# Kernel tuning notes

Hardware: AMD Instinct MI355X
Metric: run time of the kernel (lower is better)

The kernel has to match this reference:

```python
import jax, jax.numpy as jnp
import numpy as np

NEG_BIG = -9e15
ALPHA = 0.2  # leakyrelu slope


def setup_inputs() -> dict:
    key = jax.random.key(0)
    k1, k2, k3, k4 = jax.random.split(key, 4)
    N, Fin, Fout = 8192, 256, 256
    input = jax.random.normal(k1, (N, Fin), dtype=jnp.float32)
    adj = jax.random.randint(k2, (N, N), 0, 2, dtype=jnp.int32)
    W = jax.random.normal(k3, (Fin, Fout), dtype=jnp.float32) * (1.0 / np.sqrt(Fin))
    a = jax.random.normal(k4, (2 * Fout, 1), dtype=jnp.float32) * (1.0 / np.sqrt(Fout))
    return {"input": input, "adj": adj, "W": W, "a": a}


def reference(input, adj, W, a):
    # h: [N, F]
    h = input @ W
    Fout = h.shape[1]
    # Fused score: e_ij = leakyrelu(h_i . a[:F] + h_j . a[F:])
    s1 = h @ a[:Fout, 0]   # [N]
    s2 = h @ a[Fout:, 0]   # [N]
    e = s1[:, None] + s2[None, :]            # [N, N]
    e = jnp.where(e >= 0, e, ALPHA * e)      # leaky relu
    e = jnp.where(adj > 0, e, NEG_BIG)       # mask
    attention = jax.nn.softmax(e, axis=1)    # row softmax
    h_prime = attention @ h                  # [N, F]
    return jax.nn.elu(h_prime)               # concat=True -> elu
```

## Files before the change

kernel.cpp:

```cpp
#include <hip/hip_runtime.h>
#include <hip/hip_bf16.h>

#define LRALPHA 0.2f
#define LOG2E 1.4426950408889634f

typedef __attribute__((ext_vector_type(8))) short frag_ab;
typedef __attribute__((ext_vector_type(4))) float frag_cd;
typedef int   iv4 __attribute__((ext_vector_type(4)));
typedef float fv4 __attribute__((ext_vector_type(4)));
typedef int   iv2 __attribute__((ext_vector_type(2)));
typedef float fv2 __attribute__((ext_vector_type(2)));
typedef unsigned int uv4 __attribute__((ext_vector_type(4)));

static __device__ __forceinline__ unsigned short f2bf(float f) {
  __hip_bfloat16 b = __float2bfloat16(f);
  unsigned short u;
  __builtin_memcpy(&u, &b, 2);
  return u;
}

#if __has_builtin(__builtin_amdgcn_exp2f)
#define EXP2F(x) __builtin_amdgcn_exp2f(x)
#else
#define EXP2F(x) exp2f(x)
#endif

static __device__ __forceinline__ unsigned cvt_pk_bf16(float lo, float hi) {
  unsigned r;
  asm("v_cvt_pk_bf16_f32 %0, %1, %2" : "=v"(r) : "v"(lo), "v"(hi));
  return r;
}

static __device__ __forceinline__ void block_sync_lds() {
  __builtin_amdgcn_sched_barrier(0);
  asm volatile("s_waitcnt lgkmcnt(0)" ::: "memory");
  __builtin_amdgcn_s_barrier();
  __builtin_amdgcn_sched_barrier(0);
}

static __device__ __forceinline__ unsigned make_w2(iv2 ca, fv2 cv,
                                                   float s1r, float mr, float& zloc) {
  float w[2];
#pragma unroll
  for (int e = 0; e < 2; ++e) {
    float ee = s1r + cv[e];
    ee = fmaxf(ee, LRALPHA * ee);
    float ww = EXP2F(ee - mr);
    ww = ca[e] ? ww : 0.f;
    zloc += ww;
    w[e] = ww;
  }
  return cvt_pk_bf16(w[0], w[1]);
}

__global__ __launch_bounds__(256, 4) void gat_hproj(
    const float* __restrict__ X, const float* __restrict__ W,
    const float* __restrict__ avec,
    float* __restrict__ s1, float* __restrict__ s2,
    unsigned short* __restrict__ hT) {
  const int tid = threadIdx.x;
  const int row0 = blockIdx.x * 16;
  const float* Xb = X + (size_t)row0 * 256;
  const int c = tid;

  float acc[16];
#pragma unroll
  for (int r = 0; r < 16; ++r) acc[r] = 0.f;

  for (int k = 0; k < 256; k += 4) {
    const float w0 = W[(k + 0) * 256 + c];
    const float w1 = W[(k + 1) * 256 + c];
    const float w2 = W[(k + 2) * 256 + c];
    const float w3 = W[(k + 3) * 256 + c];
#pragma unroll
    for (int r = 0; r < 16; ++r) {
      acc[r] = fmaf(Xb[r * 256 + k + 0], w0, acc[r]);
      acc[r] = fmaf(Xb[r * 256 + k + 1], w1, acc[r]);
      acc[r] = fmaf(Xb[r * 256 + k + 2], w2, acc[r]);
      acc[r] = fmaf(Xb[r * 256 + k + 3], w3, acc[r]);
    }
  }

  alignas(16) unsigned short hu[16];
#pragma unroll
  for (int r = 0; r < 16; ++r) hu[r] = f2bf(acc[r]);
  uv4* hdst = (uv4*)(hT + (size_t)c * 8192 + row0);
  hdst[0] = *(const uv4*)&hu[0];
  hdst[1] = *(const uv4*)&hu[8];

  const float a1c = avec[c];
  const float a2c = avec[256 + c];
  const int lane = tid & 63, wave = tid >> 6;
  __shared__ float r1[4][16], r2[4][16];
#pragma unroll
  for (int r = 0; r < 16; ++r) {
    float v1 = acc[r] * a1c;
    float v2 = acc[r] * a2c;
#pragma unroll
    for (int off = 32; off > 0; off >>= 1) {
      v1 += __shfl_down(v1, off);
      v2 += __shfl_down(v2, off);
    }
    if (lane == 0) { r1[wave][r] = v1; r2[wave][r] = v2; }
  }
  __syncthreads();
  if (tid < 16) {
    s1[row0 + tid] = (r1[0][tid] + r1[1][tid] + r1[2][tid] + r1[3][tid]) * LOG2E;
    s2[row0 + tid] = (r2[0][tid] + r2[1][tid] + r2[2][tid] + r2[3][tid]) * LOG2E;
  }
}

__global__ __launch_bounds__(1024, 4) void gat_attn_full(
    const int* __restrict__ adj, const unsigned short* __restrict__ hT,
    const float* __restrict__ s1, const float* __restrict__ s2,
    float* __restrict__ out) {
  const int bid = blockIdx.x;
  const int row0 = bid * 32;
  const int tid = threadIdx.x;
  const int wave = tid >> 6, lane = tid & 63;
  const int ln16 = lane & 15, quad = lane >> 4;

  __shared__ __align__(16) unsigned short P[2][32][72];
  __shared__ float Zred[32][32];
  __shared__ float wred[16];
  __shared__ float Zinv[32];

  float m = -1e30f;
  for (int i = tid; i < 8192; i += 1024) m = fmaxf(m, s2[i]);
#pragma unroll
  for (int off = 32; off > 0; off >>= 1) m = fmaxf(m, __shfl_down(m, off));
  if (lane == 0) wred[wave] = m;
  __syncthreads();
  float s2m = wred[0];
#pragma unroll
  for (int wv = 1; wv < 16; ++wv) s2m = fmaxf(s2m, wred[wv]);

  const int r = tid >> 5;
  const int cg = tid & 31;
  const float s1r = s1[row0 + r];
  const float tmv = s1r + s2m;
  const float mr = tmv >= 0.f ? tmv : LRALPHA * tmv;

  const int* adjRow = adj + (size_t)(row0 + r) * 8192 + cg * 2;
  const float* s2p = s2 + cg * 2;
  const unsigned short* hTw = hT + (size_t)(wave * 16 + ln16) * 8192 + quad * 8;

  frag_cd acc[2];
  const frag_cd fz = {0.f, 0.f, 0.f, 0.f};
  acc[0] = fz; acc[1] = fz;

  float zloc = 0.f;
  const int NIT = 128;

  {
    iv2 ca = __builtin_nontemporal_load((const iv2*)adjRow);
    fv2 cv = *(const fv2*)s2p;
    *(unsigned*)&P[0][r][cg * 2] = make_w2(ca, cv, s1r, mr, zloc);
  }
  iv2 a = __builtin_nontemporal_load((const iv2*)(adjRow + 64));
  fv2 v = *(const fv2*)(s2p + 64);
  frag_ab bfC0 = *(const frag_ab*)(hTw + 0);
  frag_ab bfC1 = *(const frag_ab*)(hTw + 32);
  block_sync_lds();

  for (int jt = 0; jt < NIT; ++jt) {
    const int cur = jt & 1, nxt = cur ^ 1;

    frag_ab bfN0, bfN1;
    if (jt + 1 < NIT) {
      const size_t jn = (size_t)(jt + 1) * 64;
      bfN0 = *(const frag_ab*)(hTw + jn);
      bfN1 = *(const frag_ab*)(hTw + jn + 32);
    }

    iv2 a2; fv2 v2;
    if (jt + 2 < NIT) {
      const int o = (jt + 2) * 64;
      a2 = __builtin_nontemporal_load((const iv2*)(adjRow + o));
      v2 = *(const fv2*)(s2p + o);
    }

    if (jt + 1 < NIT) {
      *(unsigned*)&P[nxt][r][cg * 2] = make_w2(a, v, s1r, mr, zloc);
    }

    {
      frag_ab af0 = *(const frag_ab*)&P[cur][ln16][quad * 8];
      frag_ab af1 = *(const frag_ab*)&P[cur][16 + ln16][quad * 8];
      acc[0] = __builtin_amdgcn_mfma_f32_16x16x32_bf16(af0, bfC0, acc[0], 0, 0, 0);
      acc[1] = __builtin_amdgcn_mfma_f32_16x16x32_bf16(af1, bfC0, acc[1], 0, 0, 0);
      frag_ab af2 = *(const frag_ab*)&P[cur][ln16][32 + quad * 8];
      frag_ab af3 = *(const frag_ab*)&P[cur][16 + ln16][32 + quad * 8];
      acc[0] = __builtin_amdgcn_mfma_f32_16x16x32_bf16(af2, bfC1, acc[0], 0, 0, 0);
      acc[1] = __builtin_amdgcn_mfma_f32_16x16x32_bf16(af3, bfC1, acc[1], 0, 0, 0);
    }
    block_sync_lds();
    bfC0 = bfN0; bfC1 = bfN1;
    a = a2; v = v2;
  }

  Zred[r][cg] = zloc;
  __syncthreads();
  if (tid < 32) {
    float z = 0.f;
#pragma unroll
    for (int q = 0; q < 32; ++q) z += Zred[tid][q];
    Zinv[tid] = 1.f / z;
  }
  __syncthreads();

  float* outb = out + (size_t)row0 * 256;
  const int f = wave * 16 + ln16;
#pragma unroll
  for (int mi = 0; mi < 2; ++mi) {
#pragma unroll
    for (int reg = 0; reg < 4; ++reg) {
      const int grow = mi * 16 + quad * 4 + reg;
      const float vv = acc[mi][reg] * Zinv[grow];
      const float o = vv > 0.f ? vv : expm1f(vv);
      __builtin_nontemporal_store(o, outb + (size_t)grow * 256 + f);
    }
  }
}

extern "C" void kernel_launch(void* const* d_in, const int* in_sizes, int n_in,
                              void* d_out, int out_size, void* d_ws, size_t ws_size,
                              hipStream_t stream) {
  const float* X = (const float*)d_in[0];
  const int* adj = (const int*)d_in[1];
  const float* W = (const float*)d_in[2];
  const float* avec = (const float*)d_in[3];
  float* out = (float*)d_out;

  float* wsf = (float*)d_ws;
  float* s1 = wsf;
  float* s2 = wsf + 8192;
  unsigned short* hT = (unsigned short*)(wsf + 16384);

  hipLaunchKernelGGL(gat_hproj, dim3(512), dim3(256), 0, stream, X, W, avec, s1, s2, hT);
  hipLaunchKernelGGL(gat_attn_full, dim3(256), dim3(1024), 0, stream, adj, hT, s1, s2, out);
}
```

Before: 520.4 us.

## Pack adjacency into bitmask in separate pass and retile attention MFMA waves

Adds a pre-pass kernel that reads the int32 adjacency matrix with ballots and writes a 1-bit-per-entry mask. The attention kernel then reads mask words instead of int32 entries. The 256 MB adjacency still has to be read once, now in a fully parallel streaming kernel that is not coupled to the MFMA loop. The attention kernel also changes its wave tiling to 2 row groups by 8 column groups, so each wave shares one A fragment across two B tiles. This costs an extra launch and a mask write into the workspace.

```diff
diff --git a/kernel.cpp b/kernel.cpp
--- a/kernel.cpp
+++ b/kernel.cpp
@@ -6,9 +6,6 @@
 
 typedef __attribute__((ext_vector_type(8))) short frag_ab;
 typedef __attribute__((ext_vector_type(4))) float frag_cd;
-typedef int   iv4 __attribute__((ext_vector_type(4)));
-typedef float fv4 __attribute__((ext_vector_type(4)));
-typedef int   iv2 __attribute__((ext_vector_type(2)));
 typedef float fv2 __attribute__((ext_vector_type(2)));
 typedef unsigned int uv4 __attribute__((ext_vector_type(4)));
 
@@ -38,7 +35,7 @@
   __builtin_amdgcn_sched_barrier(0);
 }
 
-static __device__ __forceinline__ unsigned make_w2(iv2 ca, fv2 cv,
+static __device__ __forceinline__ unsigned make_w2(unsigned mbits, fv2 cv,
                                                    float s1r, float mr, float& zloc) {
   float w[2];
 #pragma unroll
@@ -46,11 +43,33 @@
     float ee = s1r + cv[e];
     ee = fmaxf(ee, LRALPHA * ee);
     float ww = EXP2F(ee - mr);
-    ww = ca[e] ? ww : 0.f;
+    ww = ((mbits >> e) & 1u) ? ww : 0.f;
     zloc += ww;
     w[e] = ww;
   }
   return cvt_pk_bf16(w[0], w[1]);
+}
+
+__global__ __launch_bounds__(256) void gat_adjpack(
+    const int* __restrict__ adj, unsigned long long* __restrict__ mask) {
+  const int lane = threadIdx.x & 63;
+  const int wid = (blockIdx.x * 256 + threadIdx.x) >> 6;
+  const int NW = (2048 * 256) >> 6;
+  const int NWORDS = (8192 * 8192) / 64;
+  for (int w0 = wid * 4; w0 < NWORDS; w0 += NW * 4) {
+    int v0 = __builtin_nontemporal_load(&adj[(size_t)(w0 + 0) * 64 + lane]);
+    int v1 = __builtin_nontemporal_load(&adj[(size_t)(w0 + 1) * 64 + lane]);
+    int v2 = __builtin_nontemporal_load(&adj[(size_t)(w0 + 2) * 64 + lane]);
+    int v3 = __builtin_nontemporal_load(&adj[(size_t)(w0 + 3) * 64 + lane]);
+    unsigned long long m0 = __ballot(v0 > 0);
+    unsigned long long m1 = __ballot(v1 > 0);
+    unsigned long long m2 = __ballot(v2 > 0);
+    unsigned long long m3 = __ballot(v3 > 0);
+    if (lane == 0) {
+      mask[w0 + 0] = m0; mask[w0 + 1] = m1;
+      mask[w0 + 2] = m2; mask[w0 + 3] = m3;
+    }
+  }
 }
 
 __global__ __launch_bounds__(256, 4) void gat_hproj(
@@ -111,7 +130,7 @@
 }
 
 __global__ __launch_bounds__(1024, 4) void gat_attn_full(
-    const int* __restrict__ adj, const unsigned short* __restrict__ hT,
+    const unsigned* __restrict__ mask32, const unsigned short* __restrict__ hT,
     const float* __restrict__ s1, const float* __restrict__ s2,
     float* __restrict__ out) {
   const int bid = blockIdx.x;
@@ -119,6 +138,8 @@
   const int tid = threadIdx.x;
   const int wave = tid >> 6, lane = tid & 63;
   const int ln16 = lane & 15, quad = lane >> 4;
+  const int wr = wave >> 3;
+  const int wc = wave & 7;
 
   __shared__ __align__(16) unsigned short P[2][32][72];
   __shared__ float Zred[32][32];
@@ -141,9 +162,11 @@
   const float tmv = s1r + s2m;
   const float mr = tmv >= 0.f ? tmv : LRALPHA * tmv;
 
-  const int* adjRow = adj + (size_t)(row0 + r) * 8192 + cg * 2;
+  const unsigned* mrow = mask32 + (size_t)(row0 + r) * 256 + (cg >> 4);
+  const int msh = (cg & 15) * 2;
   const float* s2p = s2 + cg * 2;
-  const unsigned short* hTw = hT + (size_t)(wave * 16 + ln16) * 8192 + quad * 8;
+  const unsigned short* hTw0 = hT + (size_t)(wc * 32 + ln16) * 8192 + quad * 8;
+  const unsigned short* hTw1 = hTw0 + (size_t)16 * 8192;
 
   frag_cd acc[2];
   const frag_cd fz = {0.f, 0.f, 0.f, 0.f};
@@ -153,50 +176,57 @@
   const int NIT = 128;
 
   {
-    iv2 ca = __builtin_nontemporal_load((const iv2*)adjRow);
+    unsigned mw = mrow[0];
     fv2 cv = *(const fv2*)s2p;
-    *(unsigned*)&P[0][r][cg * 2] = make_w2(ca, cv, s1r, mr, zloc);
-  }
-  iv2 a = __builtin_nontemporal_load((const iv2*)(adjRow + 64));
-  fv2 v = *(const fv2*)(s2p + 64);
-  frag_ab bfC0 = *(const frag_ab*)(hTw + 0);
-  frag_ab bfC1 = *(const frag_ab*)(hTw + 32);
+    *(unsigned*)&P[0][r][cg * 2] = make_w2(mw >> msh, cv, s1r, mr, zloc);
+  }
+  unsigned pm = mrow[2];
+  fv2 pv = *(const fv2*)(s2p + 64);
+  frag_ab bfC[2][2];
+#pragma unroll
+  for (int kk = 0; kk < 2; ++kk) {
+    bfC[kk][0] = *(const frag_ab*)(hTw0 + kk * 32);
+    bfC[kk][1] = *(const frag_ab*)(hTw1 + kk * 32);
+  }
   block_sync_lds();
 
   for (int jt = 0; jt < NIT; ++jt) {
     const int cur = jt & 1, nxt = cur ^ 1;
 
-    frag_ab bfN0, bfN1;
+    frag_ab bfN[2][2];
     if (jt + 1 < NIT) {
       const size_t jn = (size_t)(jt + 1) * 64;
-      bfN0 = *(const frag_ab*)(hTw + jn);
-      bfN1 = *(const frag_ab*)(hTw + jn + 32);
-    }
-
-    iv2 a2; fv2 v2;
+#pragma unroll
+      for (int kk = 0; kk < 2; ++kk) {
+        bfN[kk][0] = *(const frag_ab*)(hTw0 + jn + kk * 32);
+        bfN[kk][1] = *(const frag_ab*)(hTw1 + jn + kk * 32);
+      }
+    }
+
+    unsigned pm2 = 0; fv2 pv2;
     if (jt + 2 < NIT) {
-      const int o = (jt + 2) * 64;
-      a2 = __builtin_nontemporal_load((const iv2*)(adjRow + o));
-      v2 = *(const fv2*)(s2p + o);
+      pm2 = mrow[(jt + 2) * 2];
+      pv2 = *(const fv2*)(s2p + (jt + 2) * 64);
     }
 
     if (jt + 1 < NIT) {
-      *(unsigned*)&P[nxt][r][cg * 2] = make_w2(a, v, s1r, mr, zloc);
+      *(unsigned*)&P[nxt][r][cg * 2] = make_w2(pm >> msh, pv, s1r, mr, zloc);
     }
 
     {
-      frag_ab af0 = *(const frag_ab*)&P[cur][ln16][quad * 8];
-      frag_ab af1 = *(const frag_ab*)&P[cur][16 + ln16][quad * 8];
-      acc[0] = __builtin_amdgcn_mfma_f32_16x16x32_bf16(af0, bfC0, acc[0], 0, 0, 0);
-      acc[1] = __builtin_amdgcn_mfma_f32_16x16x32_bf16(af1, bfC0, acc[1], 0, 0, 0);
-      frag_ab af2 = *(const frag_ab*)&P[cur][ln16][32 + quad * 8];
-      frag_ab af3 = *(const frag_ab*)&P[cur][16 + ln16][32 + quad * 8];
-      acc[0] = __builtin_amdgcn_mfma_f32_16x16x32_bf16(af2, bfC1, acc[0], 0, 0, 0);
-      acc[1] = __builtin_amdgcn_mfma_f32_16x16x32_bf16(af3, bfC1, acc[1], 0, 0, 0);
+      frag_ab af0 = *(const frag_ab*)&P[cur][wr * 16 + ln16][quad * 8];
+      acc[0] = __builtin_amdgcn_mfma_f32_16x16x32_bf16(af0, bfC[0][0], acc[0], 0, 0, 0);
+      acc[1] = __builtin_amdgcn_mfma_f32_16x16x32_bf16(af0, bfC[0][1], acc[1], 0, 0, 0);
+      frag_ab af1 = *(const frag_ab*)&P[cur][wr * 16 + ln16][32 + quad * 8];
+      acc[0] = __builtin_amdgcn_mfma_f32_16x16x32_bf16(af1, bfC[1][0], acc[0], 0, 0, 0);
+      acc[1] = __builtin_amdgcn_mfma_f32_16x16x32_bf16(af1, bfC[1][1], acc[1], 0, 0, 0);
     }
     block_sync_lds();
-    bfC0 = bfN0; bfC1 = bfN1;
-    a = a2; v = v2;
+#pragma unroll
+    for (int kk = 0; kk < 2; ++kk) {
+      bfC[kk][0] = bfN[kk][0]; bfC[kk][1] = bfN[kk][1];
+    }
+    pm = pm2; pv = pv2;
   }
 
   Zred[r][cg] = zloc;
@@ -210,15 +240,15 @@
   __syncthreads();
 
   float* outb = out + (size_t)row0 * 256;
-  const int f = wave * 16 + ln16;
-#pragma unroll
-  for (int mi = 0; mi < 2; ++mi) {
+  const int f0 = wc * 32 + ln16;
+#pragma unroll
+  for (int ni = 0; ni < 2; ++ni) {
 #pragma unroll
     for (int reg = 0; reg < 4; ++reg) {
-      const int grow = mi * 16 + quad * 4 + reg;
-      const float vv = acc[mi][reg] * Zinv[grow];
+      const int grow = wr * 16 + quad * 4 + reg;
+      const float vv = acc[ni][reg] * Zinv[grow];
       const float o = vv > 0.f ? vv : expm1f(vv);
-      __builtin_nontemporal_store(o, outb + (size_t)grow * 256 + f);
+      __builtin_nontemporal_store(o, outb + (size_t)grow * 256 + f0 + ni * 16);
     }
   }
 }
@@ -236,7 +266,10 @@
   float* s1 = wsf;
   float* s2 = wsf + 8192;
   unsigned short* hT = (unsigned short*)(wsf + 16384);
-
+  unsigned long long* mask = (unsigned long long*)(wsf + 16384 + 1048576);
+
+  hipLaunchKernelGGL(gat_adjpack, dim3(2048), dim3(256), 0, stream, adj, mask);
   hipLaunchKernelGGL(gat_hproj, dim3(512), dim3(256), 0, stream, X, W, avec, s1, s2, hT);
-  hipLaunchKernelGGL(gat_attn_full, dim3(256), dim3(1024), 0, stream, adj, hT, s1, s2, out);
-}
+  hipLaunchKernelGGL(gat_attn_full, dim3(256), dim3(1024), 0, stream,
+                     (const unsigned*)mask, hT, s1, s2, out);
+}
```

Result: slower. 662.7 us (+27.4%).
